# Kernel tuning notes

Hardware: AMD Instinct MI355X
Metric: run time of the kernel (lower is better)

The kernel has to match this reference:

```python
import jax, jax.numpy as jnp
import numpy as np

C = 256
CQK = C // 8  # 32

def setup_inputs() -> dict:
    key = jax.random.key(0)
    ks = jax.random.split(key, 9)
    B, H, W = 4, 64, 64
    shp = (B, C, H, W)
    v = jax.random.normal(ks[0], shp, dtype=jnp.float32)
    k = jax.random.normal(ks[1], shp, dtype=jnp.float32)
    q = jax.random.normal(ks[2], shp, dtype=jnp.float32)
    s = 1.0 / np.sqrt(C)
    Wq = jax.random.normal(ks[3], (CQK, C), dtype=jnp.float32) * s
    bq = jnp.zeros((CQK,), dtype=jnp.float32)
    Wk = jax.random.normal(ks[4], (CQK, C), dtype=jnp.float32) * s
    bk = jnp.zeros((CQK,), dtype=jnp.float32)
    Wv = jax.random.normal(ks[5], (C, C), dtype=jnp.float32) * s
    bv = jnp.zeros((C,), dtype=jnp.float32)
    # torch inits gamma=0 (out == v); use small nonzero so attention path is exercised
    gamma = jnp.full((1,), 0.5, dtype=jnp.float32)
    return {"v": v, "k": k, "q": q, "Wq": Wq, "bq": bq, "Wk": Wk, "bk": bk,
            "Wv": Wv, "bv": bv, "gamma": gamma}

def reference(v, k, q, Wq, bq, Wk, bk, Wv, bv, gamma):
    B, Cc, Hh, Ww = v.shape
    N = Hh * Ww
    # 1x1 convs == per-pixel channel matmuls
    pq = jnp.einsum('oc,bchw->bohw', Wq, q) + bq[None, :, None, None]  # B,CQK,H,W
    pk = jnp.einsum('oc,bchw->bohw', Wk, k) + bk[None, :, None, None]
    pv = jnp.einsum('oc,bchw->bohw', Wv, v) + bv[None, :, None, None]  # B,C,H,W
    pq = pq.reshape(B, -1, N)  # B,d,N
    pk = pk.reshape(B, -1, N)
    pv = pv.reshape(B, Cc, N)
    # energy[b,n,m] = <q_n, k_m>; softmax over m (keys)
    energy = jnp.einsum('bdn,bdm->bnm', pq, pk)
    attn = jax.nn.softmax(energy, axis=-1)
    # out[b,c,n] = sum_m v[b,c,m] * attn[b,n,m]
    out = jnp.einsum('bcm,bnm->bcn', pv, attn).reshape(B, Cc, Hh, Ww)
    return gamma * out + v
```

## Files before the change

### kernel.cpp

```cpp
#include <hip/hip_runtime.h>
#include <hip/hip_bf16.h>

typedef __attribute__((ext_vector_type(8))) short short8_t;
typedef __attribute__((ext_vector_type(4))) short short4_t;
typedef __attribute__((ext_vector_type(4))) float float4_t;

#define B_   4
#define C_   256
#define N_   4096
#define DQK  32

#define VMCNT4   asm volatile("s_waitcnt vmcnt(4)" ::: "memory")
#define LGKM0    asm volatile("s_waitcnt lgkmcnt(0)" ::: "memory")
#define SBAR     __builtin_amdgcn_s_barrier()
#define SCHEDB   __builtin_amdgcn_sched_barrier(0)

__device__ __forceinline__ unsigned short f2bf(float x) {
    union { float f; unsigned int u; } v; v.f = x;
    unsigned int r = v.u + 0x7FFFu + ((v.u >> 16) & 1u);
    return (unsigned short)(r >> 16);
}
__device__ __forceinline__ unsigned short f2bf_hw(float x) {
    return __bfloat16_as_ushort(__float2bfloat16(x));
}

__global__ __launch_bounds__(256) void cast_transpose_k(
        const float* __restrict__ v_in, const float* __restrict__ k_in,
        const float* __restrict__ q_in,
        unsigned short* __restrict__ vT, unsigned short* __restrict__ kT,
        unsigned short* __restrict__ qT) {
    __shared__ float tile[32][33];
    int b = blockIdx.z & 3;
    int which = blockIdx.z >> 2;
    const float* src = which == 0 ? v_in : which == 1 ? k_in : q_in;
    unsigned short* dst = which == 0 ? vT : which == 1 ? kT : qT;
    int nb = blockIdx.x * 32, cb = blockIdx.y * 32;
    int tx = threadIdx.x, ty = threadIdx.y;
#pragma unroll
    for (int i = 0; i < 4; ++i)
        tile[ty + 8 * i][tx] = src[((size_t)(b * C_ + cb + ty + 8 * i)) * N_ + nb + tx];
    __syncthreads();
#pragma unroll
    for (int i = 0; i < 4; ++i)
        dst[((size_t)b * N_ + nb + ty + 8 * i) * C_ + cb + tx] = f2bf(tile[tx][ty + 8 * i]);
}

__global__ __launch_bounds__(256) void cast_w_k(
        const float* __restrict__ Wq, const float* __restrict__ Wk,
        const float* __restrict__ Wv,
        unsigned short* __restrict__ Wqb, unsigned short* __restrict__ Wkb,
        unsigned short* __restrict__ Wvb) {
    int i = blockIdx.x * 256 + threadIdx.x;
    if (i < 8192)            Wqb[i] = f2bf(Wq[i]);
    else if (i < 16384)      Wkb[i - 8192] = f2bf(Wk[i - 8192]);
    else                     Wvb[i - 16384] = f2bf(Wv[i - 16384]);
}

__global__ __launch_bounds__(256) void proj_qk_k(
        const unsigned short* __restrict__ qT, const unsigned short* __restrict__ kT,
        const unsigned short* __restrict__ Wqb, const unsigned short* __restrict__ Wkb,
        const float* __restrict__ bq, const float* __restrict__ bk,
        unsigned short* __restrict__ pqT, unsigned short* __restrict__ pkT) {
    int b = blockIdx.y, z = blockIdx.z;
    const unsigned short* X = z ? kT : qT;
    const unsigned short* W = z ? Wkb : Wqb;
    const float* bias = z ? bk : bq;
    unsigned short* P = z ? pkT : pqT;
    int tid = threadIdx.x, wave = tid >> 6, lane = tid & 63, l15 = lane & 15, g = lane >> 4;
    int nb = blockIdx.x * 64 + wave * 16;
    float4_t acc0 = {0.f, 0.f, 0.f, 0.f}, acc1 = {0.f, 0.f, 0.f, 0.f};
    const short8_t* Xrow = (const short8_t*)(X + ((size_t)b * N_ + nb + l15) * C_);
#pragma unroll
    for (int kk = 0; kk < 8; ++kk) {
        short8_t a  = Xrow[kk * 4 + g];
        short8_t b0 = *(const short8_t*)(W + (size_t)l15 * C_ + kk * 32 + 8 * g);
        short8_t b1 = *(const short8_t*)(W + (size_t)(16 + l15) * C_ + kk * 32 + 8 * g);
        acc0 = __builtin_amdgcn_mfma_f32_16x16x32_bf16(a, b0, acc0, 0, 0, 0);
        acc1 = __builtin_amdgcn_mfma_f32_16x16x32_bf16(a, b1, acc1, 0, 0, 0);
    }
#pragma unroll
    for (int r = 0; r < 4; ++r) {
        int n = nb + 4 * g + r;
        P[((size_t)b * N_ + n) * DQK + l15]      = f2bf(acc0[r] + bias[l15]);
        P[((size_t)b * N_ + n) * DQK + 16 + l15] = f2bf(acc1[r] + bias[16 + l15]);
    }
}

__global__ __launch_bounds__(256) void proj_v_k(
        const unsigned short* __restrict__ vT, const unsigned short* __restrict__ Wvb,
        const float* __restrict__ bv, unsigned short* __restrict__ pv) {
    int b = blockIdx.y;
    int tid = threadIdx.x, wave = tid >> 6, lane = tid & 63, l15 = lane & 15, g = lane >> 4;
    int mb = blockIdx.x * 16;
    int m = mb + l15;
    int k32 = m & 31;
    int pcol = (k32 < 16) ? ((k32 >> 2) * 8 + (k32 & 3))
                          : (((k32 - 16) >> 2) * 8 + 4 + (k32 & 3));
    int mcol = (m & ~31) + pcol;
    float4_t acc[4];
#pragma unroll
    for (int i = 0; i < 4; ++i) acc[i] = (float4_t){0.f, 0.f, 0.f, 0.f};
    const short8_t* Vrow = (const short8_t*)(vT + ((size_t)b * N_ + mb + l15) * C_);
#pragma unroll
    for (int kk = 0; kk < 8; ++kk) {
        short8_t bf = Vrow[kk * 4 + g];
#pragma unroll
        for (int ct = 0; ct < 4; ++ct) {
            short8_t af = *(const short8_t*)(Wvb + (size_t)(wave * 64 + ct * 16 + l15) * C_ + kk * 32 + 8 * g);
            acc[ct] = __builtin_amdgcn_mfma_f32_16x16x32_bf16(af, bf, acc[ct], 0, 0, 0);
        }
    }
#pragma unroll
    for (int ct = 0; ct < 4; ++ct)
#pragma unroll
        for (int r = 0; r < 4; ++r) {
            int c = wave * 64 + ct * 16 + 4 * g + r;
            pv[((size_t)b * C_ + c) * N_ + mcol] = f2bf(acc[ct][r] + bv[c]);
        }
}

__global__ __launch_bounds__(256) void attn_split_k(
        const unsigned short* __restrict__ pqT, const unsigned short* __restrict__ pkT,
        const unsigned short* __restrict__ pv,
        float* __restrict__ accP, float* __restrict__ lP, int KS) {
    __shared__ __align__(16) unsigned short VT[2][256][64];
    int nqb = gridDim.x;
    int lin = blockIdx.x + nqb * (blockIdx.y + KS * blockIdx.z);
    int cpx = (nqb * KS * 4) >> 3;
    int sl  = (lin & 7) * cpx + (lin >> 3);
    int qbi = sl % nqb;
    int s   = (sl / nqb) % KS;
    int b   = sl / (nqb * KS);

    int kps = N_ / KS, ks0 = s * kps, nt = kps >> 6;
    int tid = threadIdx.x, wave = tid >> 6, lane = tid & 63, l15 = lane & 15, g = lane >> 4;
    int qb = qbi * 64;
    int sw = (l15 & 7) << 4;
    int rl = lane >> 3, cp = lane & 7, cl = cp ^ rl;

    short8_t qf = *(const short8_t*)(pqT + ((size_t)b * N_ + qb + wave * 16 + l15) * DQK + 8 * g);
    float4_t acc[16];
#pragma unroll
    for (int i = 0; i < 16; ++i) acc[i] = (float4_t){0.f, 0.f, 0.f, 0.f};
    float l_acc = 0.f;
    const float4_t zero4 = {0.f, 0.f, 0.f, 0.f};
    const unsigned short* pvb = pv + (size_t)b * C_ * N_;

#pragma unroll
    for (int i = 0; i < 8; ++i) {
        int row0 = wave * 64 + i * 8;
        const unsigned short* src = pvb + (size_t)(row0 + rl) * N_ + ks0 + 8 * cl;
        __builtin_amdgcn_global_load_lds(
            (const __attribute__((address_space(1))) unsigned int*)(const void*)src,
            (__attribute__((address_space(3))) unsigned int*)(void*)&VT[0][row0][0], 16, 0, 0);
    }
    short8_t kfc[4];
#pragma unroll
    for (int it = 0; it < 4; ++it)
        kfc[it] = *(const short8_t*)(pkT + ((size_t)b * N_ + ks0 + 16 * it + l15) * DQK + 8 * g);
    VMCNT4; SCHEDB;
    SBAR;

    for (int t = 0; t < nt; ++t) {
        const int rb = t & 1;
        const int msn = ks0 + (t + 1) * 64;
        if (t + 1 < nt) {
#pragma unroll
            for (int i = 0; i < 8; ++i) {
                int row0 = wave * 64 + i * 8;
                const unsigned short* src = pvb + (size_t)(row0 + rl) * N_ + msn + 8 * cl;
                __builtin_amdgcn_global_load_lds(
                    (const __attribute__((address_space(1))) unsigned int*)(const void*)src,
                    (__attribute__((address_space(3))) unsigned int*)(void*)&VT[rb ^ 1][row0][0], 16, 0, 0);
            }
        }
        SCHEDB;
        float4_t sv[4];
#pragma unroll
        for (int it = 0; it < 4; ++it)
            sv[it] = __builtin_amdgcn_mfma_f32_16x16x32_bf16(kfc[it], qf, zero4, 0, 0, 0);
        short8_t kfn[4];
        if (t + 1 < nt) {
#pragma unroll
            for (int it = 0; it < 4; ++it)
                kfn[it] = *(const short8_t*)(pkT + ((size_t)b * N_ + msn + 16 * it + l15) * DQK + 8 * g);
        }
        SCHEDB;
        float p[16];
#pragma unroll
        for (int it = 0; it < 4; ++it)
#pragma unroll
            for (int r = 0; r < 4; ++r) {
                p[it * 4 + r] = __expf(sv[it][r]);
                l_acc += p[it * 4 + r];
            }
        short8_t pb0, pb1;
#pragma unroll
        for (int j = 0; j < 4; ++j) {
            pb0[j]     = (short)f2bf_hw(p[j]);
            pb0[4 + j] = (short)f2bf_hw(p[4 + j]);
            pb1[j]     = (short)f2bf_hw(p[8 + j]);
            pb1[4 + j] = (short)f2bf_hw(p[12 + j]);
        }
        const char* vb = (const char*)&VT[rb][0][0];
        __builtin_amdgcn_s_setprio(1);
#pragma unroll
        for (int ct = 0; ct < 16; ++ct) {
            const char* vrow = vb + (ct * 16 + l15) * 128;
            short8_t va0 = *(const short8_t*)(vrow + ((16 * g) ^ sw));
            short8_t va1 = *(const short8_t*)(vrow + ((64 + 16 * g) ^ sw));
            acc[ct] = __builtin_amdgcn_mfma_f32_16x16x32_bf16(va0, pb0, acc[ct], 0, 0, 0);
            acc[ct] = __builtin_amdgcn_mfma_f32_16x16x32_bf16(va1, pb1, acc[ct], 0, 0, 0);
        }
        __builtin_amdgcn_s_setprio(0);
        if (t + 1 < nt) {
            LGKM0; SCHEDB;
            SBAR;
            VMCNT4; SCHEDB;
            SBAR;
#pragma unroll
            for (int it = 0; it < 4; ++it) kfc[it] = kfn[it];
        }
    }

    l_acc += __shfl_xor(l_acc, 16);
    l_acc += __shfl_xor(l_acc, 32);
    if (g == 0)
        lP[(size_t)(b * KS + s) * N_ + qb + wave * 16 + l15] = l_acc;
    float* accOut = accP + ((size_t)(b * KS + s) * C_) * N_;
#pragma unroll
    for (int ct = 0; ct < 16; ++ct)
#pragma unroll
        for (int r = 0; r < 4; ++r) {
            int c = ct * 16 + 4 * g + r;
            accOut[(size_t)c * N_ + qb + wave * 16 + l15] = acc[ct][r];
        }
}

__global__ __launch_bounds__(256) void combine_k(
        const float* __restrict__ accP, const float* __restrict__ lP,
        const float* __restrict__ v_in, const float* __restrict__ gamma,
        float* __restrict__ out, int KS) {
    int i = blockIdx.x * 256 + threadIdx.x;
    const int nq4 = N_ / 4;
    int q0 = (i % nq4) * 4;
    int c  = (i / nq4) % C_;
    int b  = i / (nq4 * C_);
    float4_t num = {0.f, 0.f, 0.f, 0.f}, den = {0.f, 0.f, 0.f, 0.f};
    for (int s = 0; s < KS; ++s) {
        float4_t l4 = *(const float4_t*)(lP + (size_t)(b * KS + s) * N_ + q0);
        float4_t a4 = *(const float4_t*)(accP + ((size_t)(b * KS + s) * C_ + c) * N_ + q0);
#pragma unroll
        for (int j = 0; j < 4; ++j) {
            den[j] += l4[j];
            num[j] += a4[j];
        }
    }
    float gm = gamma[0];
    size_t idx = ((size_t)(b * C_ + c)) * N_ + q0;
    float4_t vi = *(const float4_t*)(v_in + idx);
    float4_t o;
#pragma unroll
    for (int j = 0; j < 4; ++j) o[j] = gm * num[j] / den[j] + vi[j];
    *(float4_t*)(out + idx) = o;
}

extern "C" void kernel_launch(void* const* d_in, const int* in_sizes, int n_in,
                              void* d_out, int out_size, void* d_ws, size_t ws_size,
                              hipStream_t stream) {
    (void)in_sizes; (void)n_in; (void)out_size;
    const float* v_in  = (const float*)d_in[0];
    const float* k_in  = (const float*)d_in[1];
    const float* q_in  = (const float*)d_in[2];
    const float* Wq    = (const float*)d_in[3];
    const float* bq    = (const float*)d_in[4];
    const float* Wk    = (const float*)d_in[5];
    const float* bk    = (const float*)d_in[6];
    const float* Wv    = (const float*)d_in[7];
    const float* bv    = (const float*)d_in[8];
    const float* gamma = (const float*)d_in[9];
    float* out = (float*)d_out;

    char* ws = (char*)d_ws;
    unsigned short* qT  = (unsigned short*)(ws + 0);
    unsigned short* kT  = (unsigned short*)(ws + 8388608);
    unsigned short* vT  = (unsigned short*)(ws + 16777216);
    unsigned short* pvb = (unsigned short*)(ws + 25165824);
    unsigned short* pqT = (unsigned short*)(ws + 33554432);
    unsigned short* pkT = (unsigned short*)(ws + 34603008);
    unsigned short* Wqb = (unsigned short*)(ws + 35651584);
    unsigned short* Wkb = (unsigned short*)(ws + 35667968);
    unsigned short* Wvb = (unsigned short*)(ws + 35684352);
    const size_t base2 = 35815424;

    int KS = 2;
    while (KS > 1) {
        size_t need = base2 + (size_t)KS * 16777216 + (size_t)KS * 262144;
        if (need <= ws_size) break;
        KS >>= 1;
    }
    float* accP = (float*)(ws + base2);
    float* lP   = (float*)(ws + base2 + (size_t)KS * 16777216);

    cast_transpose_k<<<dim3(128, 8, 12), dim3(32, 8), 0, stream>>>(v_in, k_in, q_in, vT, kT, qT);
    cast_w_k<<<320, 256, 0, stream>>>(Wq, Wk, Wv, Wqb, Wkb, Wvb);
    proj_qk_k<<<dim3(64, 4, 2), 256, 0, stream>>>(qT, kT, Wqb, Wkb, bq, bk, pqT, pkT);
    proj_v_k<<<dim3(256, 4), 256, 0, stream>>>(vT, Wvb, bv, pvb);
    attn_split_k<<<dim3(64, KS, 4), 256, 0, stream>>>(pqT, pkT, pvb, accP, lP, KS);
    combine_k<<<4096, 256, 0, stream>>>(accP, lP, v_in, gamma, out, KS);
}
```

Measured before the change: 118.1 us.

## Fuse fp32 cast into projections, use exp2 with prescaled Q, pipeline LDS reads

Removes the separate cast-transpose kernel: the projection kernels now read fp32 inputs directly in channel-major layout, convert them to bf16 in registers, and feed MFMA, avoiding a full bf16 copy of q, k and v. Q is prescaled by log2(e) so the attention loop can use exp2f, and the row-sum is computed as a tree. The V fragment LDS reads are split into groups and interleaved with the MFMAs, with launch bounds set for two blocks per CU. The fused loads are strided gathers across channels, which may coalesce poorly and raise register pressure.

```diff
diff --git a/kernel.cpp b/kernel.cpp
--- a/kernel.cpp
+++ b/kernel.cpp
@@ -9,6 +9,7 @@
 #define C_   256
 #define N_   4096
 #define DQK  32
+#define LOG2E 1.4426950408889634f
 
 #define VMCNT4   asm volatile("s_waitcnt vmcnt(4)" ::: "memory")
 #define LGKM0    asm volatile("s_waitcnt lgkmcnt(0)" ::: "memory")
@@ -22,27 +23,6 @@
 }
 __device__ __forceinline__ unsigned short f2bf_hw(float x) {
     return __bfloat16_as_ushort(__float2bfloat16(x));
-}
-
-__global__ __launch_bounds__(256) void cast_transpose_k(
-        const float* __restrict__ v_in, const float* __restrict__ k_in,
-        const float* __restrict__ q_in,
-        unsigned short* __restrict__ vT, unsigned short* __restrict__ kT,
-        unsigned short* __restrict__ qT) {
-    __shared__ float tile[32][33];
-    int b = blockIdx.z & 3;
-    int which = blockIdx.z >> 2;
-    const float* src = which == 0 ? v_in : which == 1 ? k_in : q_in;
-    unsigned short* dst = which == 0 ? vT : which == 1 ? kT : qT;
-    int nb = blockIdx.x * 32, cb = blockIdx.y * 32;
-    int tx = threadIdx.x, ty = threadIdx.y;
-#pragma unroll
-    for (int i = 0; i < 4; ++i)
-        tile[ty + 8 * i][tx] = src[((size_t)(b * C_ + cb + ty + 8 * i)) * N_ + nb + tx];
-    __syncthreads();
-#pragma unroll
-    for (int i = 0; i < 4; ++i)
-        dst[((size_t)b * N_ + nb + ty + 8 * i) * C_ + cb + tx] = f2bf(tile[tx][ty + 8 * i]);
 }
 
 __global__ __launch_bounds__(256) void cast_w_k(
@@ -57,22 +37,26 @@
 }
 
 __global__ __launch_bounds__(256) void proj_qk_k(
-        const unsigned short* __restrict__ qT, const unsigned short* __restrict__ kT,
+        const float* __restrict__ q_in, const float* __restrict__ k_in,
         const unsigned short* __restrict__ Wqb, const unsigned short* __restrict__ Wkb,
         const float* __restrict__ bq, const float* __restrict__ bk,
         unsigned short* __restrict__ pqT, unsigned short* __restrict__ pkT) {
     int b = blockIdx.y, z = blockIdx.z;
-    const unsigned short* X = z ? kT : qT;
+    const float* X = z ? k_in : q_in;
     const unsigned short* W = z ? Wkb : Wqb;
     const float* bias = z ? bk : bq;
     unsigned short* P = z ? pkT : pqT;
+    float scl = z ? 1.0f : LOG2E;
     int tid = threadIdx.x, wave = tid >> 6, lane = tid & 63, l15 = lane & 15, g = lane >> 4;
     int nb = blockIdx.x * 64 + wave * 16;
     float4_t acc0 = {0.f, 0.f, 0.f, 0.f}, acc1 = {0.f, 0.f, 0.f, 0.f};
-    const short8_t* Xrow = (const short8_t*)(X + ((size_t)b * N_ + nb + l15) * C_);
+    const float* Xcol = X + (size_t)b * C_ * N_ + nb + l15;
 #pragma unroll
     for (int kk = 0; kk < 8; ++kk) {
-        short8_t a  = Xrow[kk * 4 + g];
+        short8_t a;
+#pragma unroll
+        for (int j = 0; j < 8; ++j)
+            a[j] = (short)f2bf(Xcol[(size_t)(kk * 32 + 8 * g + j) * N_]);
         short8_t b0 = *(const short8_t*)(W + (size_t)l15 * C_ + kk * 32 + 8 * g);
         short8_t b1 = *(const short8_t*)(W + (size_t)(16 + l15) * C_ + kk * 32 + 8 * g);
         acc0 = __builtin_amdgcn_mfma_f32_16x16x32_bf16(a, b0, acc0, 0, 0, 0);
@@ -81,13 +65,13 @@
 #pragma unroll
     for (int r = 0; r < 4; ++r) {
         int n = nb + 4 * g + r;
-        P[((size_t)b * N_ + n) * DQK + l15]      = f2bf(acc0[r] + bias[l15]);
-        P[((size_t)b * N_ + n) * DQK + 16 + l15] = f2bf(acc1[r] + bias[16 + l15]);
+        P[((size_t)b * N_ + n) * DQK + l15]      = f2bf((acc0[r] + bias[l15]) * scl);
+        P[((size_t)b * N_ + n) * DQK + 16 + l15] = f2bf((acc1[r] + bias[16 + l15]) * scl);
     }
 }
 
 __global__ __launch_bounds__(256) void proj_v_k(
-        const unsigned short* __restrict__ vT, const unsigned short* __restrict__ Wvb,
+        const float* __restrict__ v_in, const unsigned short* __restrict__ Wvb,
         const float* __restrict__ bv, unsigned short* __restrict__ pv) {
     int b = blockIdx.y;
     int tid = threadIdx.x, wave = tid >> 6, lane = tid & 63, l15 = lane & 15, g = lane >> 4;
@@ -100,10 +84,13 @@
     float4_t acc[4];
 #pragma unroll
     for (int i = 0; i < 4; ++i) acc[i] = (float4_t){0.f, 0.f, 0.f, 0.f};
-    const short8_t* Vrow = (const short8_t*)(vT + ((size_t)b * N_ + mb + l15) * C_);
+    const float* Vcol = v_in + (size_t)b * C_ * N_ + mb + l15;
 #pragma unroll
     for (int kk = 0; kk < 8; ++kk) {
-        short8_t bf = Vrow[kk * 4 + g];
+        short8_t bf;
+#pragma unroll
+        for (int j = 0; j < 8; ++j)
+            bf[j] = (short)f2bf(Vcol[(size_t)(kk * 32 + 8 * g + j) * N_]);
 #pragma unroll
         for (int ct = 0; ct < 4; ++ct) {
             short8_t af = *(const short8_t*)(Wvb + (size_t)(wave * 64 + ct * 16 + l15) * C_ + kk * 32 + 8 * g);
@@ -119,7 +106,7 @@
         }
 }
 
-__global__ __launch_bounds__(256) void attn_split_k(
+__global__ __launch_bounds__(256, 2) void attn_split_k(
         const unsigned short* __restrict__ pqT, const unsigned short* __restrict__ pkT,
         const unsigned short* __restrict__ pv,
         float* __restrict__ accP, float* __restrict__ lP, int KS) {
@@ -146,6 +133,20 @@
     const float4_t zero4 = {0.f, 0.f, 0.f, 0.f};
     const unsigned short* pvb = pv + (size_t)b * C_ * N_;
 
+#define LOADG(dst, base)                                                      \
+    _Pragma("unroll")                                                         \
+    for (int i_ = 0; i_ < 4; ++i_) {                                          \
+        const char* vrow_ = vb + (((base) + i_) * 16 + l15) * 128;            \
+        dst[i_][0] = *(const short8_t*)(vrow_ + ((16 * g) ^ sw));             \
+        dst[i_][1] = *(const short8_t*)(vrow_ + ((64 + 16 * g) ^ sw));        \
+    }
+#define MFMAG(frag, ctbase)                                                   \
+    _Pragma("unroll")                                                         \
+    for (int i_ = 0; i_ < 4; ++i_) {                                          \
+        acc[(ctbase) + i_] = __builtin_amdgcn_mfma_f32_16x16x32_bf16(frag[i_][0], pb0, acc[(ctbase) + i_], 0, 0, 0); \
+        acc[(ctbase) + i_] = __builtin_amdgcn_mfma_f32_16x16x32_bf16(frag[i_][1], pb1, acc[(ctbase) + i_], 0, 0, 0); \
+    }
+
 #pragma unroll
     for (int i = 0; i < 8; ++i) {
         int row0 = wave * 64 + i * 8;
@@ -175,6 +176,10 @@
             }
         }
         SCHEDB;
+        const char* vb = (const char*)&VT[rb][0][0];
+        short8_t vg0[4][2], vg1[4][2];
+        LOADG(vg0, 0);
+        LOADG(vg1, 4);
         float4_t sv[4];
 #pragma unroll
         for (int it = 0; it < 4; ++it)
@@ -185,15 +190,17 @@
             for (int it = 0; it < 4; ++it)
                 kfn[it] = *(const short8_t*)(pkT + ((size_t)b * N_ + msn + 16 * it + l15) * DQK + 8 * g);
         }
-        SCHEDB;
         float p[16];
 #pragma unroll
         for (int it = 0; it < 4; ++it)
 #pragma unroll
-            for (int r = 0; r < 4; ++r) {
-                p[it * 4 + r] = __expf(sv[it][r]);
-                l_acc += p[it * 4 + r];
-            }
+            for (int r = 0; r < 4; ++r)
+                p[it * 4 + r] = exp2f(sv[it][r]);
+        float s0 = (p[0] + p[1]) + (p[2] + p[3]);
+        float s1 = (p[4] + p[5]) + (p[6] + p[7]);
+        float s2 = (p[8] + p[9]) + (p[10] + p[11]);
+        float s3 = (p[12] + p[13]) + (p[14] + p[15]);
+        l_acc += (s0 + s1) + (s2 + s3);
         short8_t pb0, pb1;
 #pragma unroll
         for (int j = 0; j < 4; ++j) {
@@ -202,16 +209,13 @@
             pb1[j]     = (short)f2bf_hw(p[8 + j]);
             pb1[4 + j] = (short)f2bf_hw(p[12 + j]);
         }
-        const char* vb = (const char*)&VT[rb][0][0];
         __builtin_amdgcn_s_setprio(1);
-#pragma unroll
-        for (int ct = 0; ct < 16; ++ct) {
-            const char* vrow = vb + (ct * 16 + l15) * 128;
-            short8_t va0 = *(const short8_t*)(vrow + ((16 * g) ^ sw));
-            short8_t va1 = *(const short8_t*)(vrow + ((64 + 16 * g) ^ sw));
-            acc[ct] = __builtin_amdgcn_mfma_f32_16x16x32_bf16(va0, pb0, acc[ct], 0, 0, 0);
-            acc[ct] = __builtin_amdgcn_mfma_f32_16x16x32_bf16(va1, pb1, acc[ct], 0, 0, 0);
-        }
+        MFMAG(vg0, 0);
+        LOADG(vg0, 8);
+        MFMAG(vg1, 4);
+        LOADG(vg1, 12);
+        MFMAG(vg0, 8);
+        MFMAG(vg1, 12);
         __builtin_amdgcn_s_setprio(0);
         if (t + 1 < nt) {
             LGKM0; SCHEDB;
@@ -235,6 +239,8 @@
             int c = ct * 16 + 4 * g + r;
             accOut[(size_t)c * N_ + qb + wave * 16 + l15] = acc[ct][r];
         }
+#undef LOADG
+#undef MFMAG
 }
 
 __global__ __launch_bounds__(256) void combine_k(
@@ -282,16 +288,13 @@
     float* out = (float*)d_out;
 
     char* ws = (char*)d_ws;
-    unsigned short* qT  = (unsigned short*)(ws + 0);
-    unsigned short* kT  = (unsigned short*)(ws + 8388608);
-    unsigned short* vT  = (unsigned short*)(ws + 16777216);
-    unsigned short* pvb = (unsigned short*)(ws + 25165824);
-    unsigned short* pqT = (unsigned short*)(ws + 33554432);
-    unsigned short* pkT = (unsigned short*)(ws + 34603008);
-    unsigned short* Wqb = (unsigned short*)(ws + 35651584);
-    unsigned short* Wkb = (unsigned short*)(ws + 35667968);
-    unsigned short* Wvb = (unsigned short*)(ws + 35684352);
-    const size_t base2 = 35815424;
+    unsigned short* pvb = (unsigned short*)(ws + 0);
+    unsigned short* pqT = (unsigned short*)(ws + 8388608);
+    unsigned short* pkT = (unsigned short*)(ws + 9437184);
+    unsigned short* Wqb = (unsigned short*)(ws + 10485760);
+    unsigned short* Wkb = (unsigned short*)(ws + 10502144);
+    unsigned short* Wvb = (unsigned short*)(ws + 10518528);
+    const size_t base2 = 10649600;
 
     int KS = 2;
     while (KS > 1) {
@@ -302,10 +305,9 @@
     float* accP = (float*)(ws + base2);
     float* lP   = (float*)(ws + base2 + (size_t)KS * 16777216);
 
-    cast_transpose_k<<<dim3(128, 8, 12), dim3(32, 8), 0, stream>>>(v_in, k_in, q_in, vT, kT, qT);
     cast_w_k<<<320, 256, 0, stream>>>(Wq, Wk, Wv, Wqb, Wkb, Wvb);
-    proj_qk_k<<<dim3(64, 4, 2), 256, 0, stream>>>(qT, kT, Wqb, Wkb, bq, bk, pqT, pkT);
-    proj_v_k<<<dim3(256, 4), 256, 0, stream>>>(vT, Wvb, bv, pvb);
+    proj_qk_k<<<dim3(64, 4, 2), 256, 0, stream>>>(q_in, k_in, Wqb, Wkb, bq, bk, pqT, pkT);
+    proj_v_k<<<dim3(256, 4), 256, 0, stream>>>(v_in, Wvb, bv, pvb);
     attn_split_k<<<dim3(64, KS, 4), 256, 0, stream>>>(pqT, pkT, pvb, accP, lP, KS);
     combine_k<<<4096, 256, 0, stream>>>(accP, lP, v_in, gamma, out, KS);
 }
```

New measurement: 102.3 us. 1.15x faster.
